# Optimization experiments

Hardware: AMD Instinct MI355X
Metric: run time of the kernel (lower is better)

## Reference

```python
import jax, jax.numpy as jnp
import numpy as np

NUM_USERS = 100000
NUM_ITEMS = 50000
EMBED_DIM = 64
N_LAYERS = 3
NUM_EDGES = 3276800  # avg user degree 32
BATCH = 16384


def setup_inputs() -> dict:
    key = jax.random.key(0)
    k0, k1, k2, k3, k4, k5 = jax.random.split(key, 6)
    rows = jax.random.randint(k0, (NUM_EDGES,), 0, NUM_USERS, dtype=jnp.int32)
    cols = jax.random.randint(k1, (NUM_EDGES,), 0, NUM_ITEMS, dtype=jnp.int32)
    user_table = jax.random.normal(k2, (NUM_USERS, EMBED_DIM), dtype=jnp.float32) * 0.1
    item_table = jax.random.normal(k3, (NUM_ITEMS, EMBED_DIM), dtype=jnp.float32) * 0.1
    user_indices = jax.random.randint(k4, (BATCH,), 0, NUM_USERS, dtype=jnp.int32)
    item_indices = jax.random.randint(k5, (BATCH,), 0, NUM_ITEMS, dtype=jnp.int32)
    return {
        "user_table": user_table,
        "item_table": item_table,
        "rows": rows,
        "cols": cols,
        "user_indices": user_indices,
        "item_indices": item_indices,
    }


def reference(user_table, item_table, rows, cols, user_indices, item_indices):
    # D^-1 A row-normalization of the binary bipartite adjacency:
    # normalized edge value for edge (u, i) is 1 / deg(u) (0 if isolated).
    ones = jnp.ones(rows.shape, dtype=user_table.dtype)
    deg = jax.ops.segment_sum(ones, rows, num_segments=NUM_USERS)
    inv_deg = jnp.where(deg > 0, 1.0 / deg, 0.0)
    vals = inv_deg[rows]  # [E]

    u = user_table  # [U, D] (unused by propagation in the original too)
    it = item_table  # [I, D]
    for _ in range(N_LAYERS):
        # u = A @ it  (SpMM via gather + segment-sum over destination users)
        u = jax.ops.segment_sum(vals[:, None] * it[cols], rows, num_segments=NUM_USERS)
        # it = A^T @ u
        it = jax.ops.segment_sum(vals[:, None] * u[rows], cols, num_segments=NUM_ITEMS)

    scores = jnp.sum(u[user_indices] * it[item_indices], axis=-1)  # [B]
    return jax.nn.sigmoid(scores)
```

## Files before the change

### kernel.cpp

```cpp
#include <hip/hip_runtime.h>
#include <math.h>

#define NUM_USERS 100000
#define NUM_ITEMS 50000
#define EMBED     64
#define NUM_EDGES 3276800
#define BATCH     16384
#define CAP       12800
#define NBUCK     391
#define P1_EDGES  8192
#define P1_THREADS 512
#define P2_THREADS 1024
#define CVT_GROUPS (NUM_ITEMS * 8)
#define CVT_BLOCKS ((CVT_GROUPS + P1_THREADS - 1) / P1_THREADS)

typedef _Float16 half8 __attribute__((ext_vector_type(8)));

union H8 { half8 v; int i[4]; };

__device__ __forceinline__ half8 slot_reduce(half8 acc) {
    H8 a; a.v = acc;
    H8 o;
    #pragma unroll
    for (int j = 0; j < 4; ++j) o.i[j] = __shfl_xor(a.i[j], 8, 64);
    a.v += o.v;
    #pragma unroll
    for (int j = 0; j < 4; ++j) o.i[j] = __shfl_xor(a.i[j], 16, 64);
    a.v += o.v;
    #pragma unroll
    for (int j = 0; j < 4; ++j) o.i[j] = __shfl_xor(a.i[j], 32, 64);
    a.v += o.v;
    return a.v;
}

__global__ void __launch_bounds__(P1_THREADS)
build_kernel(const int* __restrict__ rows, const int* __restrict__ cols,
             const float* __restrict__ itab, _Float16* __restrict__ it16,
             _Float16* __restrict__ w16,
             int* __restrict__ ucur, int* __restrict__ icur,
             int* __restrict__ rec_u, int* __restrict__ rec_i) {
    __shared__ int hu[400], hi[400], gu[400], gi[400];
    __shared__ int lbase[400], lcur[400];
    __shared__ int sc[512];
    __shared__ int recbuf[P1_EDGES];
    int t = threadIdx.x;

    if (blockIdx.x >= 400) {
        int b = blockIdx.x - 400;
        if (b < CVT_BLOCKS) {
            int i = b * P1_THREADS + t;
            if (i < CVT_GROUPS) {
                const float4* p = (const float4*)itab + 2 * i;
                float4 a = p[0], c = p[1];
                half8 o;
                o[0] = (_Float16)a.x; o[1] = (_Float16)a.y; o[2] = (_Float16)a.z; o[3] = (_Float16)a.w;
                o[4] = (_Float16)c.x; o[5] = (_Float16)c.y; o[6] = (_Float16)c.z; o[7] = (_Float16)c.w;
                ((half8*)it16)[i] = o;
            }
        } else {
            if (t < 64) w16[(long long)NUM_USERS * EMBED + t] = (_Float16)0.f;
            else if (t < 128) it16[(long long)NUM_ITEMS * EMBED + (t - 64)] = (_Float16)0.f;
        }
        return;
    }

    long long e0 = (long long)blockIdx.x * P1_EDGES;
    int er[16], ec[16];
    #pragma unroll
    for (int q = 0; q < 16; ++q) {
        er[q] = rows[e0 + t + q * P1_THREADS];
        ec[q] = cols[e0 + t + q * P1_THREADS];
    }

    for (int i = t; i < 400; i += P1_THREADS) { hu[i] = 0; hi[i] = 0; }
    __syncthreads();
    #pragma unroll
    for (int q = 0; q < 16; ++q) {
        atomicAdd(&hu[er[q] >> 8], 1);
        atomicAdd(&hi[ec[q] >> 7], 1);
    }
    __syncthreads();
    for (int i = t; i < 400; i += P1_THREADS) {
        int vr = (hu[i] + 15) & ~15;
        gu[i] = vr ? atomicAdd(&ucur[i], vr) : 0;
        vr = (hi[i] + 15) & ~15;
        gi[i] = vr ? atomicAdd(&icur[i], vr) : 0;
    }

    __syncthreads();
    sc[t] = (t < 400) ? hu[t] : 0;
    __syncthreads();
    for (int o = 1; o < 512; o <<= 1) {
        int x = (t >= o) ? sc[t - o] : 0; __syncthreads();
        sc[t] += x; __syncthreads();
    }
    if (t < 400) { lbase[t] = sc[t] - hu[t]; lcur[t] = 0; }
    __syncthreads();
    #pragma unroll
    for (int q = 0; q < 16; ++q) {
        int b = er[q] >> 8;
        int p = lbase[b] + atomicAdd(&lcur[b], 1);
        recbuf[p] = (ec[q] << 8) | (er[q] & 255);
    }
    __syncthreads();
    sc[t] = (t < 400) ? ((hu[t] + 15) & ~15) : 0;
    __syncthreads();
    for (int o = 1; o < 512; o <<= 1) {
        int x = (t >= o) ? sc[t - o] : 0; __syncthreads();
        sc[t] += x; __syncthreads();
    }
    int total = sc[511];
    for (int o4 = t * 4; o4 < total; o4 += P1_THREADS * 4) {
        int lo = 0, hi_ = 399;
        while (lo < hi_) { int mid = (lo + hi_) >> 1; if (sc[mid] > o4) hi_ = mid; else lo = mid + 1; }
        int b = lo;
        int v = hu[b];
        int vr = (v + 15) & ~15;
        int j = o4 - (sc[b] - vr);
        int gpos = gu[b] + j;
        if (gpos + 3 < CAP) {
            int4 val;
            val.x = (j + 0 < v) ? recbuf[lbase[b] + j + 0] : -1;
            val.y = (j + 1 < v) ? recbuf[lbase[b] + j + 1] : -1;
            val.z = (j + 2 < v) ? recbuf[lbase[b] + j + 2] : -1;
            val.w = (j + 3 < v) ? recbuf[lbase[b] + j + 3] : -1;
            *(int4*)(rec_u + (long long)b * CAP + gpos) = val;
        } else {
            for (int k = 0; k < 4; ++k)
                if (gpos + k < CAP)
                    rec_u[(long long)b * CAP + gpos + k] = (j + k < v) ? recbuf[lbase[b] + j + k] : -1;
        }
    }

    __syncthreads();
    sc[t] = (t < 400) ? hi[t] : 0;
    __syncthreads();
    for (int o = 1; o < 512; o <<= 1) {
        int x = (t >= o) ? sc[t - o] : 0; __syncthreads();
        sc[t] += x; __syncthreads();
    }
    if (t < 400) { lbase[t] = sc[t] - hi[t]; lcur[t] = 0; }
    __syncthreads();
    #pragma unroll
    for (int q = 0; q < 16; ++q) {
        int b = ec[q] >> 7;
        int p = lbase[b] + atomicAdd(&lcur[b], 1);
        recbuf[p] = (er[q] << 7) | (ec[q] & 127);
    }
    __syncthreads();
    sc[t] = (t < 400) ? ((hi[t] + 15) & ~15) : 0;
    __syncthreads();
    for (int o = 1; o < 512; o <<= 1) {
        int x = (t >= o) ? sc[t - o] : 0; __syncthreads();
        sc[t] += x; __syncthreads();
    }
    total = sc[511];
    for (int o4 = t * 4; o4 < total; o4 += P1_THREADS * 4) {
        int lo = 0, hi_ = 399;
        while (lo < hi_) { int mid = (lo + hi_) >> 1; if (sc[mid] > o4) hi_ = mid; else lo = mid + 1; }
        int b = lo;
        int v = hi[b];
        int vr = (v + 15) & ~15;
        int j = o4 - (sc[b] - vr);
        int gpos = gi[b] + j;
        if (gpos + 3 < CAP) {
            int4 val;
            val.x = (j + 0 < v) ? recbuf[lbase[b] + j + 0] : -1;
            val.y = (j + 1 < v) ? recbuf[lbase[b] + j + 1] : -1;
            val.z = (j + 2 < v) ? recbuf[lbase[b] + j + 2] : -1;
            val.w = (j + 3 < v) ? recbuf[lbase[b] + j + 3] : -1;
            *(int4*)(rec_i + (long long)b * CAP + gpos) = val;
        } else {
            for (int k = 0; k < 4; ++k)
                if (gpos + k < CAP)
                    rec_i[(long long)b * CAP + gpos + k] = (j + k < v) ? recbuf[lbase[b] + j + k] : -1;
        }
    }
}

template <int VBITS>
__device__ __forceinline__ void pass2_body(int* __restrict__ rec, const int* __restrict__ cur,
                                           int* __restrict__ deg, int* __restrict__ off,
                                           float* __restrict__ inv32, int ncap, int b, int sentinel,
                                           int* buf, int* h, int* ex, int* cnt, int* sc) {
    const int V = 1 << VBITS, M = V - 1;
    int t = threadIdx.x;
    long long s = (long long)b * CAP;
    int n = cur[b]; if (n > CAP) n = CAP;
    int nv = (n + 3) >> 2;
    const int4* rec4 = (const int4*)(rec + s);
    for (int i = t; i < nv; i += P2_THREADS) {
        int4 v4 = rec4[i];
        buf[4 * i + 0] = v4.x; buf[4 * i + 1] = v4.y;
        buf[4 * i + 2] = v4.z; buf[4 * i + 3] = v4.w;
    }
    if (t < V) { h[t] = 0; cnt[t] = 0; }
    __syncthreads();
    for (int i = t; i < n; i += P2_THREADS) {
        int r = buf[i];
        if (r != -1) atomicAdd(&h[r & M], 1);
    }
    __syncthreads();
    if (t < V) sc[t] = (h[t] + 15) & ~15;
    __syncthreads();
    for (int o = 1; o < V; o <<= 1) {
        int x = (t >= o && t < V) ? sc[t - o] : 0;
        __syncthreads();
        if (t < V) sc[t] += x;
        __syncthreads();
    }
    if (t < V) {
        int ph = (h[t] + 15) & ~15;
        int pb = sc[t] - ph;
        ex[t] = pb;
        int id = b * V + t;
        if (id < ncap) {
            int v = h[t];
            deg[id] = v;
            off[id] = (int)(s + pb);
            if (inv32) inv32[id] = v ? 1.0f / (float)v : 0.0f;
        }
        for (int j = h[t]; j < ph && pb + j < CAP; ++j) rec[s + pb + j] = sentinel;
    }
    __syncthreads();
    for (int i = t; i < n; i += P2_THREADS) {
        int r = buf[i];
        if (r == -1) continue;
        int k = r & M;
        int rnk = atomicAdd(&cnt[k], 1);
        int p = ex[k] + rnk;
        if (p < CAP)
            rec[s + p] = (int)((((unsigned)r) >> VBITS) << 7);
    }
}

__global__ void __launch_bounds__(P2_THREADS)
pass2_kernel(int* __restrict__ rec_u, const int* __restrict__ ucur,
             int* __restrict__ udeg, int* __restrict__ uoff, float* __restrict__ inv32,
             int* __restrict__ rec_i, const int* __restrict__ icur,
             int* __restrict__ ideg, int* __restrict__ ioff) {
    __shared__ int buf[CAP];
    __shared__ int h[256], ex[256], cnt[256], sc[256];
    if (blockIdx.x < NBUCK)
        pass2_body<8>(rec_u, ucur, udeg, uoff, inv32, NUM_USERS, blockIdx.x,
                      NUM_ITEMS << 7, buf, h, ex, cnt, sc);
    else
        pass2_body<7>(rec_i, icur, ideg, ioff, (float*)nullptr, NUM_ITEMS,
                      blockIdx.x - NBUCK, NUM_USERS << 7, buf, h, ex, cnt, sc);
}

__global__ void gather_u(const int* __restrict__ uoff, const int* __restrict__ udeg,
                         const int* __restrict__ csr_boff, const float* __restrict__ inv32,
                         const _Float16* __restrict__ it, _Float16* __restrict__ w) {
    int row = blockIdx.x * 4 + (threadIdx.x >> 6);
    if (row >= NUM_USERS) return;
    int lane = threadIdx.x & 63;
    int slot = lane >> 3;
    int h    = lane & 7;
    int start = uoff[row];
    int pend = start + ((udeg[row] + 15) & ~15);
    const char* itb = (const char*)it;
    unsigned hoff = (unsigned)(h << 4);
    half8 acc = {};
    int k = start;
    for (; k + 32 <= pend; k += 32) {
        int4 o4 = *(const int4*)(csr_boff + k + slot * 4);
        half8 x0 = *(const half8*)(itb + ((unsigned)o4.x + hoff));
        half8 x1 = *(const half8*)(itb + ((unsigned)o4.y + hoff));
        half8 x2 = *(const half8*)(itb + ((unsigned)o4.z + hoff));
        half8 x3 = *(const half8*)(itb + ((unsigned)o4.w + hoff));
        acc += (x0 + x1) + (x2 + x3);
    }
    if (k < pend) {
        int2 o2 = *(const int2*)(csr_boff + k + slot * 2);
        half8 x0 = *(const half8*)(itb + ((unsigned)o2.x + hoff));
        half8 x1 = *(const half8*)(itb + ((unsigned)o2.y + hoff));
        acc += x0 + x1;
    }
    half8 r = slot_reduce(acc);
    if (lane < 8) {
        float v = inv32[row];
        float v2 = v * v;
        half8 ow;
        #pragma unroll
        for (int j = 0; j < 8; ++j) ow[j] = (_Float16)((float)r[j] * v2);
        *(half8*)(w + (long long)row * EMBED + (lane << 3)) = ow;
    }
}

__global__ void gather_it(const int* __restrict__ ioff, const int* __restrict__ ideg,
                          const int* __restrict__ csc_boff,
                          const _Float16* __restrict__ w, _Float16* __restrict__ it) {
    int col = blockIdx.x * 4 + (threadIdx.x >> 6);
    if (col >= NUM_ITEMS) return;
    int lane = threadIdx.x & 63;
    int slot = lane >> 3;
    int h    = lane & 7;
    int start = ioff[col];
    int pend = start + ((ideg[col] + 15) & ~15);
    const char* wb = (const char*)w;
    unsigned hoff = (unsigned)(h << 4);
    half8 acc = {};
    int k = start;
    for (; k + 32 <= pend; k += 32) {
        int4 o4 = *(const int4*)(csc_boff + k + slot * 4);
        half8 x0 = *(const half8*)(wb + ((unsigned)o4.x + hoff));
        half8 x1 = *(const half8*)(wb + ((unsigned)o4.y + hoff));
        half8 x2 = *(const half8*)(wb + ((unsigned)o4.z + hoff));
        half8 x3 = *(const half8*)(wb + ((unsigned)o4.w + hoff));
        acc += (x0 + x1) + (x2 + x3);
    }
    if (k < pend) {
        int2 o2 = *(const int2*)(csc_boff + k + slot * 2);
        half8 x0 = *(const half8*)(wb + ((unsigned)o2.x + hoff));
        half8 x1 = *(const half8*)(wb + ((unsigned)o2.y + hoff));
        acc += x0 + x1;
    }
    half8 r = slot_reduce(acc);
    if (lane < 8)
        *(half8*)(it + (long long)col * EMBED + (lane << 3)) = r;
}

__global__ void batch_score(const int* __restrict__ ioff, const int* __restrict__ ideg,
                            const int* __restrict__ csc_boff, const _Float16* __restrict__ w,
                            const int* __restrict__ udeg,
                            const int* __restrict__ uidx, const int* __restrict__ iidx,
                            float* __restrict__ out) {
    int b = blockIdx.x * 4 + (threadIdx.x >> 6);
    if (b >= BATCH) return;
    int lane = threadIdx.x & 63;
    int col = iidx[b];
    int slot = lane >> 3;
    int h    = lane & 7;
    int start = ioff[col];
    int pend = start + ((ideg[col] + 15) & ~15);
    const char* wb = (const char*)w;
    unsigned hoff = (unsigned)(h << 4);
    half8 acc = {};
    int k = start;
    for (; k + 32 <= pend; k += 32) {
        int4 o4 = *(const int4*)(csc_boff + k + slot * 4);
        half8 x0 = *(const half8*)(wb + ((unsigned)o4.x + hoff));
        half8 x1 = *(const half8*)(wb + ((unsigned)o4.y + hoff));
        half8 x2 = *(const half8*)(wb + ((unsigned)o4.z + hoff));
        half8 x3 = *(const half8*)(wb + ((unsigned)o4.w + hoff));
        acc += (x0 + x1) + (x2 + x3);
    }
    if (k < pend) {
        int2 o2 = *(const int2*)(csc_boff + k + slot * 2);
        half8 x0 = *(const half8*)(wb + ((unsigned)o2.x + hoff));
        half8 x1 = *(const half8*)(wb + ((unsigned)o2.y + hoff));
        acc += x0 + x1;
    }
    half8 r = slot_reduce(acc);
    int ui = uidx[b];
    half8 wv = *(const half8*)(w + (long long)ui * EMBED + (h << 3));
    float p = 0.f;
    #pragma unroll
    for (int j = 0; j < 8; ++j) p += (float)r[j] * (float)wv[j];
    p += __shfl_xor(p, 1, 64);
    p += __shfl_xor(p, 2, 64);
    p += __shfl_xor(p, 4, 64);
    if (lane == 0) {
        float s = p * (float)udeg[ui];
        out[b] = 1.0f / (1.0f + expf(-s));
    }
}

extern "C" void kernel_launch(void* const* d_in, const int* in_sizes, int n_in,
                              void* d_out, int out_size, void* d_ws, size_t ws_size,
                              hipStream_t stream) {
    const float* item_table = (const float*)d_in[1];
    const int*   rows       = (const int*)d_in[2];
    const int*   cols       = (const int*)d_in[3];
    const int*   uidx       = (const int*)d_in[4];
    const int*   iidx       = (const int*)d_in[5];
    float* out = (float*)d_out;

    char* base = (char*)d_ws;
    int*   udeg  = (int*)(base + 0);
    int*   ideg  = (int*)(base +   400000);
    int*   uoff  = (int*)(base +   600000);
    int*   ioff  = (int*)(base +  1000000);
    float* inv32 = (float*)(base + 1200000);
    int*   ucur  = (int*)(base +  1600000);
    int*   icur  = (int*)(base +  1601600);
    int*   rec_u = (int*)(base +  1720320);
    int*   rec_i = (int*)(base + 22200320);
    _Float16* w16  = (_Float16*)(base + 42680320);
    _Float16* it16 = (_Float16*)(base + 55480448);

    (void)hipMemsetAsync(ucur, 0, 3200, stream);

    build_kernel<<<400 + CVT_BLOCKS + 1, P1_THREADS, 0, stream>>>(
        rows, cols, item_table, it16, w16, ucur, icur, rec_u, rec_i);
    pass2_kernel<<<NBUCK * 2, P2_THREADS, 0, stream>>>(rec_u, ucur, udeg, uoff, inv32,
                                                       rec_i, icur, ideg, ioff);

    const int ublocks = (NUM_USERS + 3) / 4;
    const int iblocks = (NUM_ITEMS + 3) / 4;
    for (int l = 0; l < 3; ++l) {
        gather_u<<<ublocks, 256, 0, stream>>>(uoff, udeg, rec_u, inv32, it16, w16);
        if (l < 2)
            gather_it<<<iblocks, 256, 0, stream>>>(ioff, ideg, rec_i, w16, it16);
    }
    batch_score<<<BATCH / 4, 256, 0, stream>>>(ioff, ideg, rec_i, w16, udeg,
                                               uidx, iidx, out);
}
```

Measured before the change: 403.2 us.

## Split item embeddings into two 32-wide halves and gather each half separately

The fp16 item table is stored as two separate half-tables of 32 columns each. gather_u now runs twice as many blocks, each handling one half, with 16 edge slots of 4 lanes instead of 8 slots of 8 lanes. Each half-table is half the size of the full table, so the random gathers in one pass hit a smaller working set that fits the cache better. The cost is that every index list is read twice, and the reduction across lanes needs an extra shuffle stage.

```diff
diff --git a/kernel.cpp b/kernel.cpp
--- a/kernel.cpp
+++ b/kernel.cpp
@@ -11,6 +11,8 @@
 #define P1_EDGES  8192
 #define P1_THREADS 512
 #define P2_THREADS 1024
+#define UB        25000
+#define IT_SH     (50001 * 32)
 #define CVT_GROUPS (NUM_ITEMS * 8)
 #define CVT_BLOCKS ((CVT_GROUPS + P1_THREADS - 1) / P1_THREADS)
 
@@ -18,7 +20,7 @@
 
 union H8 { half8 v; int i[4]; };
 
-__device__ __forceinline__ half8 slot_reduce(half8 acc) {
+__device__ __forceinline__ half8 slot_reduce8(half8 acc) {
     H8 a; a.v = acc;
     H8 o;
     #pragma unroll
@@ -33,9 +35,27 @@
     return a.v;
 }
 
+__device__ __forceinline__ half8 slot_reduce16(half8 acc) {
+    H8 a; a.v = acc;
+    H8 o;
+    #pragma unroll
+    for (int j = 0; j < 4; ++j) o.i[j] = __shfl_xor(a.i[j], 4, 64);
+    a.v += o.v;
+    #pragma unroll
+    for (int j = 0; j < 4; ++j) o.i[j] = __shfl_xor(a.i[j], 8, 64);
+    a.v += o.v;
+    #pragma unroll
+    for (int j = 0; j < 4; ++j) o.i[j] = __shfl_xor(a.i[j], 16, 64);
+    a.v += o.v;
+    #pragma unroll
+    for (int j = 0; j < 4; ++j) o.i[j] = __shfl_xor(a.i[j], 32, 64);
+    a.v += o.v;
+    return a.v;
+}
+
 __global__ void __launch_bounds__(P1_THREADS)
 build_kernel(const int* __restrict__ rows, const int* __restrict__ cols,
-             const float* __restrict__ itab, _Float16* __restrict__ it16,
+             const float* __restrict__ itab, _Float16* __restrict__ it2,
              _Float16* __restrict__ w16,
              int* __restrict__ ucur, int* __restrict__ icur,
              int* __restrict__ rec_u, int* __restrict__ rec_i) {
@@ -50,16 +70,20 @@
         if (b < CVT_BLOCKS) {
             int i = b * P1_THREADS + t;
             if (i < CVT_GROUPS) {
+                int item = i >> 3, g = i & 7;
                 const float4* p = (const float4*)itab + 2 * i;
                 float4 a = p[0], c = p[1];
                 half8 o;
                 o[0] = (_Float16)a.x; o[1] = (_Float16)a.y; o[2] = (_Float16)a.z; o[3] = (_Float16)a.w;
                 o[4] = (_Float16)c.x; o[5] = (_Float16)c.y; o[6] = (_Float16)c.z; o[7] = (_Float16)c.w;
-                ((half8*)it16)[i] = o;
+                *(half8*)(it2 + (g >> 2) * IT_SH + item * 32 + (g & 3) * 8) = o;
             }
         } else {
             if (t < 64) w16[(long long)NUM_USERS * EMBED + t] = (_Float16)0.f;
-            else if (t < 128) it16[(long long)NUM_ITEMS * EMBED + (t - 64)] = (_Float16)0.f;
+            else if (t < 128) {
+                int idx = t - 64;
+                it2[(idx >> 5) * IT_SH + 50000 * 32 + (idx & 31)] = (_Float16)0.f;
+            }
         }
         return;
     }
@@ -178,7 +202,7 @@
     }
 }
 
-template <int VBITS>
+template <int VBITS, int SHIFT>
 __device__ __forceinline__ void pass2_body(int* __restrict__ rec, const int* __restrict__ cur,
                                            int* __restrict__ deg, int* __restrict__ off,
                                            float* __restrict__ inv32, int ncap, int b, int sentinel,
@@ -230,7 +254,7 @@
         int rnk = atomicAdd(&cnt[k], 1);
         int p = ex[k] + rnk;
         if (p < CAP)
-            rec[s + p] = (int)((((unsigned)r) >> VBITS) << 7);
+            rec[s + p] = (int)((((unsigned)r) >> VBITS) << SHIFT);
     }
 }
 
@@ -242,55 +266,64 @@
     __shared__ int buf[CAP];
     __shared__ int h[256], ex[256], cnt[256], sc[256];
     if (blockIdx.x < NBUCK)
-        pass2_body<8>(rec_u, ucur, udeg, uoff, inv32, NUM_USERS, blockIdx.x,
-                      NUM_ITEMS << 7, buf, h, ex, cnt, sc);
+        pass2_body<8, 6>(rec_u, ucur, udeg, uoff, inv32, NUM_USERS, blockIdx.x,
+                         NUM_ITEMS << 6, buf, h, ex, cnt, sc);
     else
-        pass2_body<7>(rec_i, icur, ideg, ioff, (float*)nullptr, NUM_ITEMS,
-                      blockIdx.x - NBUCK, NUM_USERS << 7, buf, h, ex, cnt, sc);
+        pass2_body<7, 7>(rec_i, icur, ideg, ioff, (float*)nullptr, NUM_ITEMS,
+                         blockIdx.x - NBUCK, NUM_USERS << 7, buf, h, ex, cnt, sc);
 }
 
 __global__ void gather_u(const int* __restrict__ uoff, const int* __restrict__ udeg,
                          const int* __restrict__ csr_boff, const float* __restrict__ inv32,
-                         const _Float16* __restrict__ it, _Float16* __restrict__ w) {
-    int row = blockIdx.x * 4 + (threadIdx.x >> 6);
+                         const _Float16* __restrict__ it2, _Float16* __restrict__ w) {
+    int bb = blockIdx.x;
+    int s = 0;
+    if (bb >= UB) { s = 1; bb -= UB; }
+    int row = bb * 4 + (threadIdx.x >> 6);
     if (row >= NUM_USERS) return;
     int lane = threadIdx.x & 63;
-    int slot = lane >> 3;
-    int h    = lane & 7;
+    int slot = lane >> 2;
+    int h    = lane & 3;
     int start = uoff[row];
     int pend = start + ((udeg[row] + 15) & ~15);
-    const char* itb = (const char*)it;
+    const char* tb = (const char*)(it2 + s * IT_SH);
     unsigned hoff = (unsigned)(h << 4);
-    half8 acc = {};
+    half8 acc0 = {}, acc1 = {};
     int k = start;
-    for (; k + 32 <= pend; k += 32) {
-        int4 o4 = *(const int4*)(csr_boff + k + slot * 4);
-        half8 x0 = *(const half8*)(itb + ((unsigned)o4.x + hoff));
-        half8 x1 = *(const half8*)(itb + ((unsigned)o4.y + hoff));
-        half8 x2 = *(const half8*)(itb + ((unsigned)o4.z + hoff));
-        half8 x3 = *(const half8*)(itb + ((unsigned)o4.w + hoff));
-        acc += (x0 + x1) + (x2 + x3);
+    for (; k + 64 <= pend; k += 64) {
+        int4 o = *(const int4*)(csr_boff + k + slot * 4);
+        half8 x0 = *(const half8*)(tb + ((unsigned)o.x + hoff));
+        half8 x1 = *(const half8*)(tb + ((unsigned)o.y + hoff));
+        half8 x2 = *(const half8*)(tb + ((unsigned)o.z + hoff));
+        half8 x3 = *(const half8*)(tb + ((unsigned)o.w + hoff));
+        acc0 += x0 + x1;
+        acc1 += x2 + x3;
+    }
+    if (k + 32 <= pend) {
+        int2 o2 = *(const int2*)(csr_boff + k + slot * 2);
+        half8 x0 = *(const half8*)(tb + ((unsigned)o2.x + hoff));
+        half8 x1 = *(const half8*)(tb + ((unsigned)o2.y + hoff));
+        acc0 += x0 + x1;
+        k += 32;
     }
     if (k < pend) {
-        int2 o2 = *(const int2*)(csr_boff + k + slot * 2);
-        half8 x0 = *(const half8*)(itb + ((unsigned)o2.x + hoff));
-        half8 x1 = *(const half8*)(itb + ((unsigned)o2.y + hoff));
-        acc += x0 + x1;
-    }
-    half8 r = slot_reduce(acc);
-    if (lane < 8) {
+        int o1 = csr_boff[k + slot];
+        acc1 += *(const half8*)(tb + ((unsigned)o1 + hoff));
+    }
+    half8 r = slot_reduce16(acc0 + acc1);
+    if (lane < 4) {
         float v = inv32[row];
         float v2 = v * v;
         half8 ow;
         #pragma unroll
         for (int j = 0; j < 8; ++j) ow[j] = (_Float16)((float)r[j] * v2);
-        *(half8*)(w + (long long)row * EMBED + (lane << 3)) = ow;
+        *(half8*)(w + (long long)row * EMBED + s * 32 + (h << 3)) = ow;
     }
 }
 
 __global__ void gather_it(const int* __restrict__ ioff, const int* __restrict__ ideg,
                           const int* __restrict__ csc_boff,
-                          const _Float16* __restrict__ w, _Float16* __restrict__ it) {
+                          const _Float16* __restrict__ w, _Float16* __restrict__ it2) {
     int col = blockIdx.x * 4 + (threadIdx.x >> 6);
     if (col >= NUM_ITEMS) return;
     int lane = threadIdx.x & 63;
@@ -303,11 +336,11 @@
     half8 acc = {};
     int k = start;
     for (; k + 32 <= pend; k += 32) {
-        int4 o4 = *(const int4*)(csc_boff + k + slot * 4);
-        half8 x0 = *(const half8*)(wb + ((unsigned)o4.x + hoff));
-        half8 x1 = *(const half8*)(wb + ((unsigned)o4.y + hoff));
-        half8 x2 = *(const half8*)(wb + ((unsigned)o4.z + hoff));
-        half8 x3 = *(const half8*)(wb + ((unsigned)o4.w + hoff));
+        int4 o = *(const int4*)(csc_boff + k + slot * 4);
+        half8 x0 = *(const half8*)(wb + ((unsigned)o.x + hoff));
+        half8 x1 = *(const half8*)(wb + ((unsigned)o.y + hoff));
+        half8 x2 = *(const half8*)(wb + ((unsigned)o.z + hoff));
+        half8 x3 = *(const half8*)(wb + ((unsigned)o.w + hoff));
         acc += (x0 + x1) + (x2 + x3);
     }
     if (k < pend) {
@@ -316,9 +349,9 @@
         half8 x1 = *(const half8*)(wb + ((unsigned)o2.y + hoff));
         acc += x0 + x1;
     }
-    half8 r = slot_reduce(acc);
+    half8 r = slot_reduce8(acc);
     if (lane < 8)
-        *(half8*)(it + (long long)col * EMBED + (lane << 3)) = r;
+        *(half8*)(it2 + (h >> 2) * IT_SH + col * 32 + (h & 3) * 8) = r;
 }
 
 __global__ void batch_score(const int* __restrict__ ioff, const int* __restrict__ ideg,
@@ -339,11 +372,11 @@
     half8 acc = {};
     int k = start;
     for (; k + 32 <= pend; k += 32) {
-        int4 o4 = *(const int4*)(csc_boff + k + slot * 4);
-        half8 x0 = *(const half8*)(wb + ((unsigned)o4.x + hoff));
-        half8 x1 = *(const half8*)(wb + ((unsigned)o4.y + hoff));
-        half8 x2 = *(const half8*)(wb + ((unsigned)o4.z + hoff));
-        half8 x3 = *(const half8*)(wb + ((unsigned)o4.w + hoff));
+        int4 o = *(const int4*)(csc_boff + k + slot * 4);
+        half8 x0 = *(const half8*)(wb + ((unsigned)o.x + hoff));
+        half8 x1 = *(const half8*)(wb + ((unsigned)o.y + hoff));
+        half8 x2 = *(const half8*)(wb + ((unsigned)o.z + hoff));
+        half8 x3 = *(const half8*)(wb + ((unsigned)o.w + hoff));
         acc += (x0 + x1) + (x2 + x3);
     }
     if (k < pend) {
@@ -352,7 +385,7 @@
         half8 x1 = *(const half8*)(wb + ((unsigned)o2.y + hoff));
         acc += x0 + x1;
     }
-    half8 r = slot_reduce(acc);
+    half8 r = slot_reduce8(acc);
     int ui = uidx[b];
     half8 wv = *(const half8*)(w + (long long)ui * EMBED + (h << 3));
     float p = 0.f;
@@ -387,22 +420,21 @@
     int*   icur  = (int*)(base +  1601600);
     int*   rec_u = (int*)(base +  1720320);
     int*   rec_i = (int*)(base + 22200320);
-    _Float16* w16  = (_Float16*)(base + 42680320);
-    _Float16* it16 = (_Float16*)(base + 55480448);
+    _Float16* w16 = (_Float16*)(base + 42680320);
+    _Float16* it2 = (_Float16*)(base + 55480448);
 
     (void)hipMemsetAsync(ucur, 0, 3200, stream);
 
     build_kernel<<<400 + CVT_BLOCKS + 1, P1_THREADS, 0, stream>>>(
-        rows, cols, item_table, it16, w16, ucur, icur, rec_u, rec_i);
+        rows, cols, item_table, it2, w16, ucur, icur, rec_u, rec_i);
     pass2_kernel<<<NBUCK * 2, P2_THREADS, 0, stream>>>(rec_u, ucur, udeg, uoff, inv32,
                                                        rec_i, icur, ideg, ioff);
 
-    const int ublocks = (NUM_USERS + 3) / 4;
     const int iblocks = (NUM_ITEMS + 3) / 4;
     for (int l = 0; l < 3; ++l) {
-        gather_u<<<ublocks, 256, 0, stream>>>(uoff, udeg, rec_u, inv32, it16, w16);
+        gather_u<<<2 * UB, 256, 0, stream>>>(uoff, udeg, rec_u, inv32, it2, w16);
         if (l < 2)
-            gather_it<<<iblocks, 256, 0, stream>>>(ioff, ideg, rec_i, w16, it16);
+            gather_it<<<iblocks, 256, 0, stream>>>(ioff, ideg, rec_i, w16, it2);
     }
     batch_score<<<BATCH / 4, 256, 0, stream>>>(ioff, ideg, rec_i, w16, udeg,
                                                uidx, iidx, out);
```

After: 478.6 us. 18.7% more time.
